# Optimization experiments

Measured on AMD Instinct MI355X. Metric: run time of the kernel, lower is better.

## Reference

```python
import jax, jax.numpy as jnp
from jax import lax
import numpy as np

T, B, INP, HS, OUT = 512, 64, 512, 2048, 512
DECAY_CENTER, DECAY_SIGMA = 1024.0, 256.0


def _decay_init(hs, center, sigma):
    # scaled bell distribution capped at its value at 2*sigma
    idx = jnp.arange(hs, dtype=jnp.float32)
    bell = jnp.exp(-((idx - center) ** 2) / (2.0 * sigma ** 2))
    cap = jnp.exp(jnp.float32(-2.0))  # value at 2 sigma from center
    return jnp.maximum(bell, cap)


def setup_inputs() -> dict:
    key = jax.random.key(0)
    ks = jax.random.split(key, 10)
    s_in = 1.0 / np.sqrt(INP)
    s_hs = 1.0 / np.sqrt(HS)
    return {
        "data": jax.random.normal(ks[0], (T, B, INP), jnp.float32),
        "Wih": jax.random.uniform(ks[1], (HS, INP), jnp.float32, -s_hs, s_hs),
        "bih": jax.random.uniform(ks[2], (HS,), jnp.float32, -s_hs, s_hs),
        "Whh": jax.random.uniform(ks[3], (HS, HS), jnp.float32, -s_hs, s_hs),
        "bhh": jax.random.uniform(ks[4], (HS,), jnp.float32, -s_hs, s_hs),
        "Wp": jax.random.uniform(ks[5], (HS, HS), jnp.float32, -s_hs, s_hs),
        "bp": jax.random.uniform(ks[6], (HS,), jnp.float32, -s_hs, s_hs),
        "decay": _decay_init(HS, DECAY_CENTER, DECAY_SIGMA),
        "Wout": jax.random.uniform(ks[7], (OUT, HS), jnp.float32, -s_hs, s_hs),
        "bout": jax.random.uniform(ks[8], (OUT,), jnp.float32, -s_hs, s_hs),
    }


def reference(data, Wih, bih, Whh, bhh, Wp, bp, decay, Wout, bout):
    Bsz = data.shape[1]
    hs = Whh.shape[0]

    def step(carry, x):
        h, pot = carry  # [B, HS] each
        # RNNCell: tanh(x W_ih^T + b_ih + h W_hh^T + b_hh)
        r = jnp.tanh(x @ Wih.T + bih + h @ Whh.T + bhh)
        # PGLU: potential accumulate + relu gate + decayed residual potential
        p = pot + r @ Wp.T + bp
        act = jax.nn.relu(p)
        pot_new = (p - act) * decay
        return (act, pot_new), None

    init = (jnp.zeros((Bsz, hs), data.dtype), jnp.zeros((Bsz, hs), data.dtype))
    (act_last, _), _ = lax.scan(step, init, data)
    return act_last @ Wout.T + bout  # [B, OUT]
```

## Files before the change

### kernel.cpp

```cpp
#include <hip/hip_runtime.h>
#include <math.h>

#define T_DIM   512
#define B_DIM   64
#define INP_DIM 512
#define HS_DIM  2048
#define OUT_DIM 512

static __device__ float g_dataT[(size_t)T_DIM * INP_DIM * B_DIM];
static __device__ float g_prex[(size_t)T_DIM * HS_DIM * B_DIM];
static __device__ float g_hT4[HS_DIM * B_DIM];
static __device__ float g_rT4[HS_DIM * B_DIM];
static __device__ float g_potT[HS_DIM * B_DIM];

__device__ __forceinline__ void async_ld16(const float* g, float* l) {
    __builtin_amdgcn_global_load_lds(
        (const __attribute__((address_space(1))) void*)g,
        (__attribute__((address_space(3))) void*)l, 16, 0, 0);
}

__global__ __launch_bounds__(256) void zero_state_kernel() {
    int i = blockIdx.x * 256 + threadIdx.x;
    if (i < HS_DIM * B_DIM) { g_hT4[i] = 0.f; g_potT[i] = 0.f; }
}

__global__ __launch_bounds__(256) void transpose_data_kernel(const float* __restrict__ data) {
    __shared__ float tile[64][65];
    const int t = blockIdx.x;
    const float* src = data + (size_t)t * B_DIM * INP_DIM;
    float* dst = g_dataT + (size_t)t * INP_DIM * B_DIM;
    for (int kt = 0; kt < INP_DIM / 64; ++kt) {
        const int k0 = kt * 64;
        __syncthreads();
        for (int i = threadIdx.x; i < 64 * 64; i += 256) {
            int b = i >> 6, kk = i & 63;
            tile[b][kk] = src[b * INP_DIM + k0 + kk];
        }
        __syncthreads();
        for (int i = threadIdx.x; i < 64 * 64; i += 256) {
            int k = i >> 6, b2 = i & 63;
            dst[(size_t)(k0 + k) * B_DIM + b2] = tile[b2][k];
        }
    }
}

__global__ __launch_bounds__(256) void prex_kernel(const float* __restrict__ Wih,
                                                   const float* __restrict__ bih,
                                                   const float* __restrict__ bhh) {
    __shared__ float lds[128 * B_DIM];
    const int t = blockIdx.y;
    const int lane = threadIdx.x & 63;
    const int wv = __builtin_amdgcn_readfirstlane(threadIdx.x >> 6);
    const int j0 = blockIdx.x * 32 + wv * 8;
    const float* xT = g_dataT + (size_t)t * INP_DIM * B_DIM;
    float acc[8] = {};
    for (int k0 = 0; k0 < INP_DIM; k0 += 128) {
        __syncthreads();
        {
            const float4* s4 = (const float4*)(xT + (size_t)k0 * B_DIM);
            float4* d4 = (float4*)lds;
            for (int i = threadIdx.x; i < 128 * B_DIM / 4; i += 256) d4[i] = s4[i];
        }
        __syncthreads();
        for (int k = 0; k < 128; k += 4) {
            float w[8][4];
            #pragma unroll
            for (int c = 0; c < 8; ++c)
                #pragma unroll
                for (int u = 0; u < 4; ++u)
                    w[c][u] = Wih[(size_t)(j0 + c) * INP_DIM + k0 + k + u];
            #pragma unroll
            for (int u = 0; u < 4; ++u) {
                float hv = lds[(k + u) * B_DIM + lane];
                #pragma unroll
                for (int c = 0; c < 8; ++c) acc[c] += hv * w[c][u];
            }
        }
    }
    #pragma unroll
    for (int c = 0; c < 8; ++c) {
        int j = j0 + c;
        g_prex[((size_t)t * HS_DIM + j) * B_DIM + lane] = acc[c] + bih[j] + bhh[j];
    }
}

template <int PHASE>
__global__ __launch_bounds__(256) void step_kernel(const float* __restrict__ W,
                                                   const float* __restrict__ bp,
                                                   const float* __restrict__ decay,
                                                   int t) {
    __shared__ float lds[16384 + 2048];
    const int lane = threadIdx.x & 63;
    const int wv = __builtin_amdgcn_readfirstlane(threadIdx.x >> 6);
    const int j0 = blockIdx.x * 8;
    const float* src = (PHASE == 0) ? g_hT4 : g_rT4;
    const int kbase4 = wv * 128;
    float* myl = &lds[wv * 4096];

    float acc[8] = {};

    #pragma unroll
    for (int r = 0; r < 8; ++r)
        async_ld16(src + (size_t)(kbase4 + r) * 256 + lane * 4, myl + r * 256);

    for (int ch = 0; ch < 16; ++ch) {
        asm volatile("s_waitcnt vmcnt(0)" ::: "memory");
        if (ch < 15) {
            float* nl = myl + (((ch + 1) & 1) << 11);
            #pragma unroll
            for (int r = 0; r < 8; ++r)
                async_ld16(src + (size_t)(kbase4 + (ch + 1) * 8 + r) * 256 + lane * 4,
                           nl + r * 256);
        }
        const float* cl = myl + ((ch & 1) << 11);
        const float* Wk = W + (size_t)j0 * HS_DIM + (size_t)(kbase4 + ch * 8) * 4;
        #pragma unroll
        for (int r = 0; r < 8; ++r) {
            float4 h4 = *(const float4*)(cl + r * 256 + lane * 4);
            #pragma unroll
            for (int c = 0; c < 8; ++c) {
                const float* w = Wk + (size_t)c * HS_DIM + r * 4;
                acc[c] = fmaf(h4.x, w[0], acc[c]);
                acc[c] = fmaf(h4.y, w[1], acc[c]);
                acc[c] = fmaf(h4.z, w[2], acc[c]);
                acc[c] = fmaf(h4.w, w[3], acc[c]);
            }
        }
    }

    float* red = &lds[16384];
    #pragma unroll
    for (int c = 0; c < 8; ++c) red[(wv * 8 + c) * 64 + lane] = acc[c];
    __syncthreads();

    #pragma unroll
    for (int s = 0; s < 2; ++s) {
        int idx = threadIdx.x + s * 256;
        int c = idx >> 6, b = idx & 63;
        int j = j0 + c;
        float sum = red[(0 * 8 + c) * 64 + b] + red[(1 * 8 + c) * 64 + b] +
                    red[(2 * 8 + c) * 64 + b] + red[(3 * 8 + c) * 64 + b];
        if (PHASE == 0) {
            float rr = tanhf(g_prex[((size_t)t * HS_DIM + j) * B_DIM + b] + sum);
            g_rT4[(size_t)(j >> 2) * 256 + b * 4 + (j & 3)] = rr;
        } else {
            float p = g_potT[(size_t)j * B_DIM + b] + sum + bp[j];
            g_hT4[(size_t)(j >> 2) * 256 + b * 4 + (j & 3)] = fmaxf(p, 0.f);
            g_potT[(size_t)j * B_DIM + b] = fminf(p, 0.f) * decay[j];
        }
    }
}

__global__ __launch_bounds__(256) void out_kernel(const float* __restrict__ Wout,
                                                  const float* __restrict__ bout,
                                                  float* __restrict__ out) {
    const int lane = threadIdx.x & 63;
    const int wv = __builtin_amdgcn_readfirstlane(threadIdx.x >> 6);
    const int o0 = blockIdx.x * 16 + wv * 4;
    float acc[4] = {};
    for (int k4 = 0; k4 < HS_DIM / 4; ++k4) {
        float4 h4 = *(const float4*)&g_hT4[(size_t)k4 * 256 + lane * 4];
        #pragma unroll
        for (int c = 0; c < 4; ++c) {
            const float* w = Wout + (size_t)(o0 + c) * HS_DIM + (size_t)k4 * 4;
            acc[c] = fmaf(h4.x, w[0], acc[c]);
            acc[c] = fmaf(h4.y, w[1], acc[c]);
            acc[c] = fmaf(h4.z, w[2], acc[c]);
            acc[c] = fmaf(h4.w, w[3], acc[c]);
        }
    }
    #pragma unroll
    for (int c = 0; c < 4; ++c)
        out[(size_t)lane * OUT_DIM + o0 + c] = acc[c] + bout[o0 + c];
}

extern "C" void kernel_launch(void* const* d_in, const int* in_sizes, int n_in,
                              void* d_out, int out_size, void* d_ws, size_t ws_size,
                              hipStream_t stream) {
    const float* data  = (const float*)d_in[0];
    const float* Wih   = (const float*)d_in[1];
    const float* bih   = (const float*)d_in[2];
    const float* Whh   = (const float*)d_in[3];
    const float* bhh   = (const float*)d_in[4];
    const float* Wp    = (const float*)d_in[5];
    const float* bp    = (const float*)d_in[6];
    const float* decay = (const float*)d_in[7];
    const float* Wout  = (const float*)d_in[8];
    const float* bout  = (const float*)d_in[9];
    float* out = (float*)d_out;

    zero_state_kernel<<<(HS_DIM * B_DIM + 255) / 256, 256, 0, stream>>>();
    transpose_data_kernel<<<T_DIM, 256, 0, stream>>>(data);
    prex_kernel<<<dim3(HS_DIM / 32, T_DIM), 256, 0, stream>>>(Wih, bih, bhh);
    for (int t = 0; t < T_DIM; ++t) {
        step_kernel<0><<<HS_DIM / 8, 256, 0, stream>>>(Whh, bp, decay, t);
        step_kernel<1><<<HS_DIM / 8, 256, 0, stream>>>(Wp, bp, decay, t);
    }
    out_kernel<<<OUT_DIM / 16, 256, 0, stream>>>(Wout, bout, out);
}
```

Measured before the change: 55.23 ms.

## Replace per-step kernel launches with a persistent cooperative kernel

Swaps the 1024 per-timestep kernel launches for one cooperative persistent kernel with 256 blocks that loops over time and uses grid.sync between the two recurrent GEMM phases. Each block keeps its 8 rows of Whh and Wp resident in LDS for the whole run, and the potential state stays in registers. The aim is to remove launch overhead and the repeated reloading of weights from global memory at every step. In exchange it pays two grid-wide barriers per step, runs at one block per CU, and falls back to the old launch path if the cooperative launch fails.

```diff
diff --git a/kernel.cpp b/kernel.cpp
--- a/kernel.cpp
+++ b/kernel.cpp
@@ -1,5 +1,8 @@
 #include <hip/hip_runtime.h>
+#include <hip/hip_cooperative_groups.h>
 #include <math.h>
+
+namespace cg = cooperative_groups;
 
 #define T_DIM   512
 #define B_DIM   64
@@ -84,6 +87,114 @@
     }
 }
 
+__device__ __forceinline__ void eighth_gemm(float acc[8], const float* __restrict__ srcT4,
+                                            const float* __restrict__ wl,
+                                            int kq4, int lane) {
+    const float4* gp = (const float4*)srcT4 + (size_t)kq4 * 64 + lane;
+    float4 bufA[8], bufB[8];
+    #pragma unroll
+    for (int r = 0; r < 8; ++r) bufA[r] = gp[r * 64];
+    #pragma unroll 1
+    for (int ch = 0; ch < 8; ch += 2) {
+        #pragma unroll
+        for (int r = 0; r < 8; ++r) bufB[r] = gp[((ch + 1) * 8 + r) * 64];
+        #pragma unroll
+        for (int r = 0; r < 8; ++r) {
+            const float4 h4 = bufA[r];
+            const int k = (kq4 + ch * 8 + r) * 4;
+            #pragma unroll
+            for (int c = 0; c < 8; ++c) {
+                const float4 w = *(const float4*)&wl[c * HS_DIM + k];
+                acc[c] = fmaf(h4.x, w.x, acc[c]);
+                acc[c] = fmaf(h4.y, w.y, acc[c]);
+                acc[c] = fmaf(h4.z, w.z, acc[c]);
+                acc[c] = fmaf(h4.w, w.w, acc[c]);
+            }
+        }
+        if (ch + 2 < 8) {
+            #pragma unroll
+            for (int r = 0; r < 8; ++r) bufA[r] = gp[((ch + 2) * 8 + r) * 64];
+        }
+        #pragma unroll
+        for (int r = 0; r < 8; ++r) {
+            const float4 h4 = bufB[r];
+            const int k = (kq4 + (ch + 1) * 8 + r) * 4;
+            #pragma unroll
+            for (int c = 0; c < 8; ++c) {
+                const float4 w = *(const float4*)&wl[c * HS_DIM + k];
+                acc[c] = fmaf(h4.x, w.x, acc[c]);
+                acc[c] = fmaf(h4.y, w.y, acc[c]);
+                acc[c] = fmaf(h4.z, w.z, acc[c]);
+                acc[c] = fmaf(h4.w, w.w, acc[c]);
+            }
+        }
+    }
+}
+
+__global__ __launch_bounds__(512, 1) void rnn_persistent(const float* __restrict__ Whh,
+                                                         const float* __restrict__ Wp,
+                                                         const float* __restrict__ bp,
+                                                         const float* __restrict__ decay) {
+    __shared__ float w_hh[8 * HS_DIM];
+    __shared__ float w_p[8 * HS_DIM];
+    __shared__ float red[8 * 8 * 64];
+
+    const int j0 = blockIdx.x * 8;
+    const int lane = threadIdx.x & 63;
+    const int wv = threadIdx.x >> 6;
+    const int kq4 = wv * 64;
+
+    {
+        const float4* A = (const float4*)(Whh + (size_t)j0 * HS_DIM);
+        const float4* B = (const float4*)(Wp + (size_t)j0 * HS_DIM);
+        float4* a = (float4*)w_hh;
+        float4* b = (float4*)w_p;
+        for (int i = threadIdx.x; i < 8 * HS_DIM / 4; i += 512) { a[i] = A[i]; b[i] = B[i]; }
+    }
+    const int jj = j0 + wv;
+    const float bpv = bp[jj];
+    const float dev = decay[jj];
+    const size_t rt4_idx = (size_t)(jj >> 2) * 256 + lane * 4 + (jj & 3);
+    float pot = 0.f;
+    __syncthreads();
+
+    cg::grid_group grid = cg::this_grid();
+
+    for (int t = 0; t < T_DIM; ++t) {
+        {
+            float acc[8] = {};
+            eighth_gemm(acc, g_hT4, w_hh, kq4, lane);
+            #pragma unroll
+            for (int c = 0; c < 8; ++c) red[(wv * 8 + c) * 64 + lane] = acc[c];
+            __syncthreads();
+            float s = 0.f;
+            #pragma unroll
+            for (int w = 0; w < 8; ++w) s += red[(w * 8 + wv) * 64 + lane];
+            float rr = tanhf(g_prex[((size_t)t * HS_DIM + jj) * B_DIM + lane] + s);
+            g_rT4[rt4_idx] = rr;
+        }
+        __threadfence();
+        grid.sync();
+        __threadfence();
+        {
+            float acc[8] = {};
+            eighth_gemm(acc, g_rT4, w_p, kq4, lane);
+            #pragma unroll
+            for (int c = 0; c < 8; ++c) red[(wv * 8 + c) * 64 + lane] = acc[c];
+            __syncthreads();
+            float s = 0.f;
+            #pragma unroll
+            for (int w = 0; w < 8; ++w) s += red[(w * 8 + wv) * 64 + lane];
+            float p = pot + s + bpv;
+            g_hT4[rt4_idx] = fmaxf(p, 0.f);
+            pot = fminf(p, 0.f) * dev;
+        }
+        __threadfence();
+        grid.sync();
+        __threadfence();
+    }
+}
+
 template <int PHASE>
 __global__ __launch_bounds__(256) void step_kernel(const float* __restrict__ W,
                                                    const float* __restrict__ bp,
@@ -98,7 +209,6 @@
     float* myl = &lds[wv * 4096];
 
     float acc[8] = {};
-
     #pragma unroll
     for (int r = 0; r < 8; ++r)
         async_ld16(src + (size_t)(kbase4 + r) * 256 + lane * 4, myl + r * 256);
@@ -192,9 +302,16 @@
     zero_state_kernel<<<(HS_DIM * B_DIM + 255) / 256, 256, 0, stream>>>();
     transpose_data_kernel<<<T_DIM, 256, 0, stream>>>(data);
     prex_kernel<<<dim3(HS_DIM / 32, T_DIM), 256, 0, stream>>>(Wih, bih, bhh);
-    for (int t = 0; t < T_DIM; ++t) {
-        step_kernel<0><<<HS_DIM / 8, 256, 0, stream>>>(Whh, bp, decay, t);
-        step_kernel<1><<<HS_DIM / 8, 256, 0, stream>>>(Wp, bp, decay, t);
-    }
+
+    void* kargs[] = {(void*)&Whh, (void*)&Wp, (void*)&bp, (void*)&decay};
+    hipError_t ce = hipLaunchCooperativeKernel((void*)rnn_persistent, dim3(256), dim3(512),
+                                               kargs, 0, stream);
+    if (ce != hipSuccess) {
+        for (int t = 0; t < T_DIM; ++t) {
+            step_kernel<0><<<HS_DIM / 8, 256, 0, stream>>>(Whh, bp, decay, t);
+            step_kernel<1><<<HS_DIM / 8, 256, 0, stream>>>(Wp, bp, decay, t);
+        }
+    }
+
     out_kernel<<<OUT_DIM / 16, 256, 0, stream>>>(Wout, bout, out);
 }
```

Result: slower. 202.0 ms (+265.8%).

## Replace per-step kernel launches with persistent kernel and grid barrier

Applied to the files above, without the earlier changes.

The 1024 per-timestep launches are replaced by one persistent kernel of 256 blocks. Each block keeps its 8 rows of Whh and Wp resident in LDS and holds the potential state in registers. Steps are separated by an atomic-counter grid barrier instead of kernel boundaries, which removes launch overhead and the repeated global reads of the weights and potential. The design relies on all 256 blocks being co-resident (one per CU on MI355X) and on relaxed atomics for visibility of the state; if blocks are not all resident, the barrier deadlocks.

```diff
diff --git a/kernel.cpp b/kernel.cpp
--- a/kernel.cpp
+++ b/kernel.cpp
@@ -11,17 +11,12 @@
 static __device__ float g_prex[(size_t)T_DIM * HS_DIM * B_DIM];
 static __device__ float g_hT4[HS_DIM * B_DIM];
 static __device__ float g_rT4[HS_DIM * B_DIM];
-static __device__ float g_potT[HS_DIM * B_DIM];
-
-__device__ __forceinline__ void async_ld16(const float* g, float* l) {
-    __builtin_amdgcn_global_load_lds(
-        (const __attribute__((address_space(1))) void*)g,
-        (__attribute__((address_space(3))) void*)l, 16, 0, 0);
-}
+static __device__ unsigned g_bar;
 
 __global__ __launch_bounds__(256) void zero_state_kernel() {
     int i = blockIdx.x * 256 + threadIdx.x;
-    if (i < HS_DIM * B_DIM) { g_hT4[i] = 0.f; g_potT[i] = 0.f; }
+    if (i < HS_DIM * B_DIM) g_hT4[i] = 0.f;
+    if (i == 0) g_bar = 0u;
 }
 
 __global__ __launch_bounds__(256) void transpose_data_kernel(const float* __restrict__ data) {
@@ -84,70 +79,127 @@
     }
 }
 
-template <int PHASE>
-__global__ __launch_bounds__(256) void step_kernel(const float* __restrict__ W,
-                                                   const float* __restrict__ bp,
-                                                   const float* __restrict__ decay,
-                                                   int t) {
-    __shared__ float lds[16384 + 2048];
-    const int lane = threadIdx.x & 63;
-    const int wv = __builtin_amdgcn_readfirstlane(threadIdx.x >> 6);
-    const int j0 = blockIdx.x * 8;
-    const float* src = (PHASE == 0) ? g_hT4 : g_rT4;
-    const int kbase4 = wv * 128;
-    float* myl = &lds[wv * 4096];
-
-    float acc[8] = {};
-
-    #pragma unroll
-    for (int r = 0; r < 8; ++r)
-        async_ld16(src + (size_t)(kbase4 + r) * 256 + lane * 4, myl + r * 256);
-
-    for (int ch = 0; ch < 16; ++ch) {
-        asm volatile("s_waitcnt vmcnt(0)" ::: "memory");
-        if (ch < 15) {
-            float* nl = myl + (((ch + 1) & 1) << 11);
-            #pragma unroll
-            for (int r = 0; r < 8; ++r)
-                async_ld16(src + (size_t)(kbase4 + (ch + 1) * 8 + r) * 256 + lane * 4,
-                           nl + r * 256);
-        }
-        const float* cl = myl + ((ch & 1) << 11);
-        const float* Wk = W + (size_t)j0 * HS_DIM + (size_t)(kbase4 + ch * 8) * 4;
+#define LD_ST8(dst, base, ro)                                                              \
+    {                                                                                      \
+        _Pragma("unroll") for (int r = 0; r < 8; ++r) {                                    \
+            dst[2 * r] = __hip_atomic_load(base + (size_t)((ro) + r) * 128,                \
+                                           __ATOMIC_RELAXED, __HIP_MEMORY_SCOPE_AGENT);    \
+            dst[2 * r + 1] = __hip_atomic_load(base + (size_t)((ro) + r) * 128 + 1,        \
+                                               __ATOMIC_RELAXED, __HIP_MEMORY_SCOPE_AGENT);\
+        }                                                                                  \
+    }
+
+__device__ __forceinline__ void eighth_gemm(float acc[8], const float* __restrict__ srcT4,
+                                            const float* __restrict__ wl,
+                                            int kq4, int lane) {
+    const unsigned long long* gp =
+        (const unsigned long long*)srcT4 + (((size_t)kq4 * 64 + lane) << 1);
+    unsigned long long bufA[16], bufB[16];
+    LD_ST8(bufA, gp, 0);
+    #pragma unroll 1
+    for (int ch = 0; ch < 8; ch += 2) {
+        LD_ST8(bufB, gp, (ch + 1) * 8);
         #pragma unroll
         for (int r = 0; r < 8; ++r) {
-            float4 h4 = *(const float4*)(cl + r * 256 + lane * 4);
+            const float2 hlo = __builtin_bit_cast(float2, bufA[2 * r]);
+            const float2 hhi = __builtin_bit_cast(float2, bufA[2 * r + 1]);
+            const int k = (kq4 + ch * 8 + r) * 4;
             #pragma unroll
             for (int c = 0; c < 8; ++c) {
-                const float* w = Wk + (size_t)c * HS_DIM + r * 4;
-                acc[c] = fmaf(h4.x, w[0], acc[c]);
-                acc[c] = fmaf(h4.y, w[1], acc[c]);
-                acc[c] = fmaf(h4.z, w[2], acc[c]);
-                acc[c] = fmaf(h4.w, w[3], acc[c]);
+                const float4 w = *(const float4*)&wl[c * HS_DIM + k];
+                acc[c] = fmaf(hlo.x, w.x, acc[c]);
+                acc[c] = fmaf(hlo.y, w.y, acc[c]);
+                acc[c] = fmaf(hhi.x, w.z, acc[c]);
+                acc[c] = fmaf(hhi.y, w.w, acc[c]);
             }
         }
-    }
-
-    float* red = &lds[16384];
-    #pragma unroll
-    for (int c = 0; c < 8; ++c) red[(wv * 8 + c) * 64 + lane] = acc[c];
+        if (ch + 2 < 8) LD_ST8(bufA, gp, (ch + 2) * 8);
+        #pragma unroll
+        for (int r = 0; r < 8; ++r) {
+            const float2 hlo = __builtin_bit_cast(float2, bufB[2 * r]);
+            const float2 hhi = __builtin_bit_cast(float2, bufB[2 * r + 1]);
+            const int k = (kq4 + (ch + 1) * 8 + r) * 4;
+            #pragma unroll
+            for (int c = 0; c < 8; ++c) {
+                const float4 w = *(const float4*)&wl[c * HS_DIM + k];
+                acc[c] = fmaf(hlo.x, w.x, acc[c]);
+                acc[c] = fmaf(hlo.y, w.y, acc[c]);
+                acc[c] = fmaf(hhi.x, w.z, acc[c]);
+                acc[c] = fmaf(hhi.y, w.w, acc[c]);
+            }
+        }
+    }
+}
+
+__device__ __forceinline__ void gbar(unsigned target) {
+    asm volatile("s_waitcnt vmcnt(0)" ::: "memory");
     __syncthreads();
-
-    #pragma unroll
-    for (int s = 0; s < 2; ++s) {
-        int idx = threadIdx.x + s * 256;
-        int c = idx >> 6, b = idx & 63;
-        int j = j0 + c;
-        float sum = red[(0 * 8 + c) * 64 + b] + red[(1 * 8 + c) * 64 + b] +
-                    red[(2 * 8 + c) * 64 + b] + red[(3 * 8 + c) * 64 + b];
-        if (PHASE == 0) {
-            float rr = tanhf(g_prex[((size_t)t * HS_DIM + j) * B_DIM + b] + sum);
-            g_rT4[(size_t)(j >> 2) * 256 + b * 4 + (j & 3)] = rr;
-        } else {
-            float p = g_potT[(size_t)j * B_DIM + b] + sum + bp[j];
-            g_hT4[(size_t)(j >> 2) * 256 + b * 4 + (j & 3)] = fmaxf(p, 0.f);
-            g_potT[(size_t)j * B_DIM + b] = fminf(p, 0.f) * decay[j];
-        }
+    if (threadIdx.x == 0) {
+        __hip_atomic_fetch_add(&g_bar, 1u, __ATOMIC_RELAXED, __HIP_MEMORY_SCOPE_AGENT);
+        while (__hip_atomic_load(&g_bar, __ATOMIC_RELAXED, __HIP_MEMORY_SCOPE_AGENT) < target)
+            __builtin_amdgcn_s_sleep(2);
+    }
+    __syncthreads();
+}
+
+__global__ __launch_bounds__(512, 1) void rnn_persistent(const float* __restrict__ Whh,
+                                                         const float* __restrict__ Wp,
+                                                         const float* __restrict__ bp,
+                                                         const float* __restrict__ decay) {
+    __shared__ float w_hh[8 * HS_DIM];
+    __shared__ float w_p[8 * HS_DIM];
+    __shared__ float red[8 * 8 * 64];
+
+    const int j0 = blockIdx.x * 8;
+    const int lane = threadIdx.x & 63;
+    const int wv = threadIdx.x >> 6;
+    const int kq4 = wv * 64;
+
+    {
+        const float4* A = (const float4*)(Whh + (size_t)j0 * HS_DIM);
+        const float4* B = (const float4*)(Wp + (size_t)j0 * HS_DIM);
+        float4* a = (float4*)w_hh;
+        float4* b = (float4*)w_p;
+        for (int i = threadIdx.x; i < 8 * HS_DIM / 4; i += 512) { a[i] = A[i]; b[i] = B[i]; }
+    }
+    const int jj = j0 + wv;
+    const float bpv = bp[jj];
+    const float dev = decay[jj];
+    const size_t st_idx = (size_t)(jj >> 2) * 256 + lane * 4 + (jj & 3);
+    float pot = 0.f;
+    unsigned nbar = 0;
+    __syncthreads();
+
+    for (int t = 0; t < T_DIM; ++t) {
+        {
+            float acc[8] = {};
+            eighth_gemm(acc, g_hT4, w_hh, kq4, lane);
+            #pragma unroll
+            for (int c = 0; c < 8; ++c) red[(wv * 8 + c) * 64 + lane] = acc[c];
+            __syncthreads();
+            float s = 0.f;
+            #pragma unroll
+            for (int w = 0; w < 8; ++w) s += red[(w * 8 + wv) * 64 + lane];
+            float rr = tanhf(g_prex[((size_t)t * HS_DIM + jj) * B_DIM + lane] + s);
+            __hip_atomic_store(&g_rT4[st_idx], rr, __ATOMIC_RELAXED, __HIP_MEMORY_SCOPE_AGENT);
+            __syncthreads();
+        }
+        gbar(++nbar * 256u);
+        {
+            float acc[8] = {};
+            eighth_gemm(acc, g_rT4, w_p, kq4, lane);
+            #pragma unroll
+            for (int c = 0; c < 8; ++c) red[(wv * 8 + c) * 64 + lane] = acc[c];
+            __syncthreads();
+            float s = 0.f;
+            #pragma unroll
+            for (int w = 0; w < 8; ++w) s += red[(w * 8 + wv) * 64 + lane];
+            float p = pot + s + bpv;
+            __hip_atomic_store(&g_hT4[st_idx], fmaxf(p, 0.f), __ATOMIC_RELAXED, __HIP_MEMORY_SCOPE_AGENT);
+            pot = fminf(p, 0.f) * dev;
+            __syncthreads();
+        }
+        gbar(++nbar * 256u);
     }
 }
 
@@ -192,9 +244,6 @@
     zero_state_kernel<<<(HS_DIM * B_DIM + 255) / 256, 256, 0, stream>>>();
     transpose_data_kernel<<<T_DIM, 256, 0, stream>>>(data);
     prex_kernel<<<dim3(HS_DIM / 32, T_DIM), 256, 0, stream>>>(Wih, bih, bhh);
-    for (int t = 0; t < T_DIM; ++t) {
-        step_kernel<0><<<HS_DIM / 8, 256, 0, stream>>>(Whh, bp, decay, t);
-        step_kernel<1><<<HS_DIM / 8, 256, 0, stream>>>(Wp, bp, decay, t);
-    }
+    rnn_persistent<<<dim3(256), dim3(512), 0, stream>>>(Whh, Wp, bp, decay);
     out_kernel<<<OUT_DIM / 16, 256, 0, stream>>>(Wout, bout, out);
 }
```

New measurement: 133.1 ms. 141% more time.
